# Performance work log

Hardware: AMD Instinct MI355X
Metric: run time of the kernel (lower is better)

The kernel has to match this reference:

```python
import jax, jax.numpy as jnp
import numpy as np

N = 50000        # nodes
E = 800000       # edges (avg degree 16)
IN = 256         # in_size
H = 4            # heads
C = 32           # out_size per head
NEG_SLOPE = 0.2  # PyG GATConv leaky_relu slope
LN_EPS = 1e-5


def setup_inputs() -> dict:
    key = jax.random.key(0)
    ks = jax.random.split(key, 6)
    x = jax.random.normal(ks[0], (N, IN), dtype=jnp.float32)
    edge_index = jax.random.randint(ks[1], (2, E), 0, N, dtype=jnp.int32)
    W = jax.random.normal(ks[2], (IN, H * C), dtype=jnp.float32) * 0.05
    att_src = jax.random.normal(ks[3], (H, C), dtype=jnp.float32) * 0.05
    att_dst = jax.random.normal(ks[4], (H, C), dtype=jnp.float32) * 0.05
    bias = jnp.zeros((H * C,), dtype=jnp.float32)
    ln_gamma = jnp.ones((H * C,), dtype=jnp.float32)
    ln_beta = jnp.zeros((H * C,), dtype=jnp.float32)
    return {"x": x, "edge_index": edge_index, "W": W, "att_src": att_src,
            "att_dst": att_dst, "bias": bias, "ln_gamma": ln_gamma,
            "ln_beta": ln_beta}


def _segment_softmax(alpha, seg, num_segments):
    # alpha: [E, H], softmax over edges sharing the same destination node.
    amax = jax.ops.segment_max(alpha, seg, num_segments=num_segments)  # [N, H]
    amax = jnp.where(jnp.isfinite(amax), amax, 0.0)  # nodes with no in-edges
    ex = jnp.exp(alpha - amax[seg])
    denom = jax.ops.segment_sum(ex, seg, num_segments=num_segments)    # [N, H]
    return ex / (denom[seg] + 1e-16)


def reference(x, edge_index, W, att_src, att_dst, bias, ln_gamma, ln_beta):
    # --- GATConv (concat=True) ---
    x_lin = (x @ W).reshape(N, H, C)                    # [N, H, C]
    a_src = jnp.sum(x_lin * att_src, axis=-1)           # [N, H]
    a_dst = jnp.sum(x_lin * att_dst, axis=-1)           # [N, H]
    src, dst = edge_index[0], edge_index[1]             # messages src -> dst
    alpha = a_src[src] + a_dst[dst]                     # [E, H]
    alpha = jnp.where(alpha >= 0, alpha, NEG_SLOPE * alpha)
    alpha = _segment_softmax(alpha, dst, N)             # [E, H]
    msg = x_lin[src] * alpha[..., None]                 # [E, H, C]
    out = jax.ops.segment_sum(msg, dst, num_segments=N) # [N, H, C]
    out = out.reshape(N, H * C) + bias                  # [N, H*C]
    # --- LayerNorm over feature dim ---
    mu = jnp.mean(out, axis=-1, keepdims=True)
    var = jnp.mean(jnp.square(out - mu), axis=-1, keepdims=True)
    out = (out - mu) * jax.lax.rsqrt(var + LN_EPS) * ln_gamma + ln_beta
    # --- activation ---
    return jax.nn.relu(out)
```

## Files before the change

kernel.cpp:

```cpp
#include <hip/hip_runtime.h>

#define NNODES 50000
#define NEDGES 800000
#define INFEAT 256
#define HC 128
#define NH 4
#define CPH 32
#define LSTRIDE 264
#define WSTR 68

typedef unsigned int uint32;
typedef unsigned short u16;
typedef short short8 __attribute__((ext_vector_type(8)));
typedef float f32x4 __attribute__((ext_vector_type(4)));

__device__ __forceinline__ float b2f(u16 s) {
    uint32 u = ((uint32)s) << 16;
    return __builtin_bit_cast(float, u);
}
__device__ __forceinline__ u16 f2bf(float x) {
    uint32 u = __builtin_bit_cast(uint32, x);
    uint32 r = (u + 0x7FFFu + ((u >> 16) & 1u)) >> 16;
    return (u16)r;
}
__device__ __forceinline__ bool probe_bf16(const void* gamma) {
    return ((const uint32*)gamma)[0] == 0x3F803F80u;
}
__device__ __forceinline__ float expleaky(float a) {
    return __expf(fmaxf(a, 0.2f * a));
}

__global__ __launch_bounds__(256) void wtp_kernel(const void* __restrict__ W,
                                                  const void* __restrict__ gm,
                                                  u16* __restrict__ wtp,
                                                  int* __restrict__ count) {
    const bool isbf = probe_bf16(gm);
    int c = blockIdx.x * 256 + threadIdx.x;
    if (c < 4096) {
        int kt = c >> 9, nt = (c >> 6) & 7, l = c & 63;
        int r = l & 15, quad = l >> 4;
        int n = nt * 16 + r;
        int kbase = kt * 32 + quad * 8;
        u16 vals[8];
#pragma unroll
        for (int j = 0; j < 8; ++j) {
            int k = kbase + j;
            vals[j] = isbf ? ((const u16*)W)[k * HC + n] : f2bf(((const float*)W)[k * HC + n]);
        }
        *(uint4*)(wtp + (size_t)c * 8) = *(const uint4*)vals;
    }
    uint4 z = {0u, 0u, 0u, 0u};
    uint4* cz = (uint4*)count;
    for (int i = c; i < NNODES / 4; i += 64 * 256) cz[i] = z;
}

__global__ __launch_bounds__(256) void gemm_mfma(const void* __restrict__ x,
                                                 const uint4* __restrict__ wtp,
                                                 const void* __restrict__ att_src,
                                                 const void* __restrict__ att_dst,
                                                 const void* __restrict__ gm,
                                                 u16* __restrict__ xlin,
                                                 float* __restrict__ asrc,
                                                 float* __restrict__ adst,
                                                 const int* __restrict__ ei,
                                                 int* __restrict__ count,
                                                 int* __restrict__ rank) {
    __shared__ u16 atile[4 * 16 * LSTRIDE];
    const bool isbf = probe_bf16(gm);
    const int tid = threadIdx.x;
    const int wv = tid >> 6;
    const int lane = tid & 63;
    int wave = blockIdx.x * 4 + wv;
    int r = lane & 15;
    int quad = lane >> 4;
    int m0 = wave * 16;
    u16* my = atile + wv * (16 * LSTRIDE);

    const int eb = blockIdx.x * 1024 + tid;
    int rnk[4];
    bool ev[4];
#pragma unroll
    for (int rep = 0; rep < 4; ++rep) ev[rep] = (eb + rep * 256) < NEDGES;

    if (isbf) {
        uint4 st[8];
#pragma unroll
        for (int rep = 0; rep < 8; ++rep) {
            int idx = rep * 64 + lane;
            int row = idx >> 5;
            int ch  = idx & 31;
            int gr = m0 + row;
            if (gr > NNODES - 1) gr = NNODES - 1;
            st[rep] = *(const uint4*)((const u16*)x + (size_t)gr * INFEAT + ch * 8);
        }
        int dsti[4];
#pragma unroll
        for (int rep = 0; rep < 4; ++rep)
            dsti[rep] = ev[rep] ? ei[NEDGES + eb + rep * 256] : 0;
#pragma unroll
        for (int rep = 0; rep < 4; ++rep)
            rnk[rep] = ev[rep] ? atomicAdd(&count[dsti[rep]], 1) : 0;
#pragma unroll
        for (int rep = 0; rep < 8; ++rep) {
            int idx = rep * 64 + lane;
            int row = idx >> 5;
            int ch  = idx & 31;
            *(uint4*)(my + row * LSTRIDE + ch * 8) = st[rep];
        }
    } else {
#pragma unroll
        for (int rep = 0; rep < 16; ++rep) {
            int idx = rep * 64 + lane;
            int row = idx >> 6;
            int c4  = idx & 63;
            int gr = m0 + row;
            if (gr > NNODES - 1) gr = NNODES - 1;
            float4 f = *(const float4*)((const float*)x + (size_t)gr * INFEAT + c4 * 4);
            u16 v[4] = {f2bf(f.x), f2bf(f.y), f2bf(f.z), f2bf(f.w)};
            *(uint2*)(my + row * LSTRIDE + c4 * 4) = *(const uint2*)v;
        }
        int dsti[4];
#pragma unroll
        for (int rep = 0; rep < 4; ++rep)
            dsti[rep] = ev[rep] ? ei[NEDGES + eb + rep * 256] : 0;
#pragma unroll
        for (int rep = 0; rep < 4; ++rep)
            rnk[rep] = ev[rep] ? atomicAdd(&count[dsti[rep]], 1) : 0;
    }

    f32x4 acc[8];
#pragma unroll
    for (int nt = 0; nt < 8; ++nt) acc[nt] = (f32x4){0.f, 0.f, 0.f, 0.f};

#pragma unroll
    for (int kt = 0; kt < 8; ++kt) {
        short8 afrag = __builtin_bit_cast(short8,
            *(const uint4*)(my + r * LSTRIDE + kt * 32 + quad * 8));
#pragma unroll
        for (int nt = 0; nt < 8; ++nt) {
            short8 bfrag = __builtin_bit_cast(short8, wtp[(kt * 8 + nt) * 64 + lane]);
            acc[nt] = __builtin_amdgcn_mfma_f32_16x16x32_bf16(afrag, bfrag, acc[nt], 0, 0, 0);
        }
    }
#pragma unroll
    for (int nt = 0; nt < 8; ++nt) {
#pragma unroll
        for (int reg = 0; reg < 4; ++reg) {
            int grow = m0 + quad * 4 + reg;
            if (grow < NNODES) xlin[(size_t)grow * HC + nt * 16 + r] = f2bf(acc[nt][reg]);
        }
    }

    float asv[8], adv[8];
#pragma unroll
    for (int nt = 0; nt < 8; ++nt) {
        int c = nt * 16 + r;
        if (isbf) {
            asv[nt] = b2f(((const u16*)att_src)[c]);
            adv[nt] = b2f(((const u16*)att_dst)[c]);
        } else {
            asv[nt] = ((const float*)att_src)[c];
            adv[nt] = ((const float*)att_dst)[c];
        }
    }
    float psrc[4][4], pdst[4][4];
#pragma unroll
    for (int h = 0; h < 4; ++h)
#pragma unroll
        for (int reg = 0; reg < 4; ++reg) { psrc[h][reg] = 0.f; pdst[h][reg] = 0.f; }
#pragma unroll
    for (int nt = 0; nt < 8; ++nt) {
        const int h = nt >> 1;
#pragma unroll
        for (int reg = 0; reg < 4; ++reg) {
            psrc[h][reg] = fmaf(acc[nt][reg], asv[nt], psrc[h][reg]);
            pdst[h][reg] = fmaf(acc[nt][reg], adv[nt], pdst[h][reg]);
        }
    }
#pragma unroll
    for (int m = 1; m < 16; m <<= 1) {
#pragma unroll
        for (int h = 0; h < 4; ++h)
#pragma unroll
            for (int reg = 0; reg < 4; ++reg) {
                psrc[h][reg] += __shfl_xor(psrc[h][reg], m);
                pdst[h][reg] += __shfl_xor(pdst[h][reg], m);
            }
    }
#pragma unroll
    for (int reg = 0; reg < 4; ++reg)
#pragma unroll
        for (int h = 0; h < 4; ++h)
            if (r == reg * 4 + h) {
                int grow = m0 + quad * 4 + reg;
                if (grow < NNODES) {
                    asrc[grow * 4 + h] = psrc[h][reg];
                    adst[grow * 4 + h] = pdst[h][reg];
                }
            }

#pragma unroll
    for (int rep = 0; rep < 4; ++rep)
        if (ev[rep]) rank[eb + rep * 256] = rnk[rep];
}

__global__ __launch_bounds__(256) void blkred_kernel(const int* __restrict__ count,
                                                     int* __restrict__ blksum) {
    int i = blockIdx.x * 256 + threadIdx.x;
    int v = (i < NNODES) ? count[i] : 0;
#pragma unroll
    for (int m = 1; m < 64; m <<= 1) v += __shfl_xor(v, m);
    __shared__ int s[4];
    if ((threadIdx.x & 63) == 0) s[threadIdx.x >> 6] = v;
    __syncthreads();
    if (threadIdx.x == 0) blksum[blockIdx.x] = s[0] + s[1] + s[2] + s[3];
}

__global__ __launch_bounds__(256) void scanout_kernel(const int* __restrict__ count,
                                                      const int* __restrict__ blksum,
                                                      int* __restrict__ offsets) {
    __shared__ int sb[256];
    __shared__ int sd[256];
    const int nblk = (NNODES + 255) / 256;
    int t = threadIdx.x;
    int bv = (t < nblk) ? blksum[t] : 0;
    sb[t] = bv;
    __syncthreads();
    for (int off = 1; off < 256; off <<= 1) {
        int tv = (t >= off) ? sb[t - off] : 0;
        __syncthreads();
        sb[t] += tv;
        __syncthreads();
    }
    int base = sb[blockIdx.x] - blksum[blockIdx.x];

    int i = blockIdx.x * 256 + t;
    int v = (i < NNODES) ? count[i] : 0;
    sd[t] = v;
    __syncthreads();
    for (int off = 1; off < 256; off <<= 1) {
        int tv = (t >= off) ? sd[t - off] : 0;
        __syncthreads();
        sd[t] += tv;
        __syncthreads();
    }
    if (i < NNODES) offsets[i] = base + sd[t] - v;
    if (i == 0) offsets[NNODES] = NEDGES;
}

__global__ __launch_bounds__(256) void scatter_kernel(const int* __restrict__ ei,
                                                      const int* __restrict__ offsets,
                                                      const int* __restrict__ rank,
                                                      int* __restrict__ col) {
    int e = blockIdx.x * 256 + threadIdx.x;
    if (e >= NEDGES) return;
    int d = ei[NEDGES + e];
    col[offsets[d] + rank[e]] = ei[e];
}

__global__ __launch_bounds__(256) void node_kernel(const u16* __restrict__ xlin,
                                                   const float* __restrict__ asrc,
                                                   const float* __restrict__ adst,
                                                   const int* __restrict__ offsets,
                                                   const int* __restrict__ col,
                                                   const void* __restrict__ bias,
                                                   const void* __restrict__ gamma,
                                                   const void* __restrict__ beta,
                                                   void* __restrict__ out) {
    __shared__ float wlds[4][4 * WSTR];
    __shared__ int   slds[4][64];
    const bool isbf = probe_bf16(gamma);
    const int wv = threadIdx.x >> 6;
    const int lane = threadIdx.x & 63;
    int node = blockIdx.x * 4 + wv;
    int h = lane >> 4;
    int f2 = lane * 2;
    int start = offsets[node];
    int end = offsets[node + 1];
    float4 ad4 = *(const float4*)(adst + (size_t)node * 4);

    float dsum = 0.f, acc0 = 0.f, acc1 = 0.f;
    float* wmy = wlds[wv];
    int* smy = slds[wv];

    for (int base = start; base < end; base += 64) {
        int cnt = end - base;
        if (cnt > 64) cnt = 64;
        float4 w4 = {0.f, 0.f, 0.f, 0.f};
        int src = 0;
        if (lane < cnt) {
            src = col[base + lane];
            float4 as4 = *(const float4*)(asrc + (size_t)src * 4);
            w4.x = expleaky(as4.x + ad4.x);
            w4.y = expleaky(as4.y + ad4.y);
            w4.z = expleaky(as4.z + ad4.z);
            w4.w = expleaky(as4.w + ad4.w);
        }
        smy[lane] = src;
        wmy[0 * WSTR + lane] = w4.x;
        wmy[1 * WSTR + lane] = w4.y;
        wmy[2 * WSTR + lane] = w4.z;
        wmy[3 * WSTR + lane] = w4.w;

        const float* wh = wmy + h * WSTR;
        int j = 0;
        for (; j + 7 < cnt; j += 8) {
            float4 wa = *(const float4*)(wh + j);
            float4 wb = *(const float4*)(wh + j + 4);
            int4 sa = *(const int4*)(smy + j);
            int4 sb = *(const int4*)(smy + j + 4);
            uint32 pf[8];
            pf[0] = *(const uint32*)(xlin + (size_t)sa.x * HC + f2);
            pf[1] = *(const uint32*)(xlin + (size_t)sa.y * HC + f2);
            pf[2] = *(const uint32*)(xlin + (size_t)sa.z * HC + f2);
            pf[3] = *(const uint32*)(xlin + (size_t)sa.w * HC + f2);
            pf[4] = *(const uint32*)(xlin + (size_t)sb.x * HC + f2);
            pf[5] = *(const uint32*)(xlin + (size_t)sb.y * HC + f2);
            pf[6] = *(const uint32*)(xlin + (size_t)sb.z * HC + f2);
            pf[7] = *(const uint32*)(xlin + (size_t)sb.w * HC + f2);
            float wv8[8] = {wa.x, wa.y, wa.z, wa.w, wb.x, wb.y, wb.z, wb.w};
#pragma unroll
            for (int k = 0; k < 8; ++k) {
                float w = wv8[k];
                dsum += w;
                float x0 = __builtin_bit_cast(float, pf[k] << 16);
                float x1 = __builtin_bit_cast(float, pf[k] & 0xffff0000u);
                acc0 = fmaf(x0, w, acc0);
                acc1 = fmaf(x1, w, acc1);
            }
        }
        for (; j + 3 < cnt; j += 4) {
            float4 wa = *(const float4*)(wh + j);
            int4 sa = *(const int4*)(smy + j);
            uint32 pf[4];
            pf[0] = *(const uint32*)(xlin + (size_t)sa.x * HC + f2);
            pf[1] = *(const uint32*)(xlin + (size_t)sa.y * HC + f2);
            pf[2] = *(const uint32*)(xlin + (size_t)sa.z * HC + f2);
            pf[3] = *(const uint32*)(xlin + (size_t)sa.w * HC + f2);
            float wv4[4] = {wa.x, wa.y, wa.z, wa.w};
#pragma unroll
            for (int k = 0; k < 4; ++k) {
                float w = wv4[k];
                dsum += w;
                float x0 = __builtin_bit_cast(float, pf[k] << 16);
                float x1 = __builtin_bit_cast(float, pf[k] & 0xffff0000u);
                acc0 = fmaf(x0, w, acc0);
                acc1 = fmaf(x1, w, acc1);
            }
        }
        for (; j < cnt; ++j) {
            float w = wh[j];
            int c = smy[j];
            uint32 p = *(const uint32*)(xlin + (size_t)c * HC + f2);
            dsum += w;
            float x0 = __builtin_bit_cast(float, p << 16);
            float x1 = __builtin_bit_cast(float, p & 0xffff0000u);
            acc0 = fmaf(x0, w, acc0);
            acc1 = fmaf(x1, w, acc1);
        }
    }
    float rden = 1.f / (dsum + 1e-16f);

    float bi0, bi1, g0, g1, be0, be1;
    if (isbf) {
        uint32 bb = ((const uint32*)bias)[lane];
        uint32 gg = ((const uint32*)gamma)[lane];
        uint32 eb = ((const uint32*)beta)[lane];
        bi0 = b2f((u16)(bb & 0xffffu)); bi1 = b2f((u16)(bb >> 16));
        g0  = b2f((u16)(gg & 0xffffu)); g1  = b2f((u16)(gg >> 16));
        be0 = b2f((u16)(eb & 0xffffu)); be1 = b2f((u16)(eb >> 16));
    } else {
        float2 tb = ((const float2*)bias)[lane];
        float2 tg = ((const float2*)gamma)[lane];
        float2 te = ((const float2*)beta)[lane];
        bi0 = tb.x; bi1 = tb.y; g0 = tg.x; g1 = tg.y; be0 = te.x; be1 = te.y;
    }
    float v0 = fmaf(acc0, rden, bi0);
    float v1 = fmaf(acc1, rden, bi1);
    float s2 = v0 + v1;
    float q2 = v0 * v0 + v1 * v1;
#pragma unroll
    for (int m = 1; m < 64; m <<= 1) {
        s2 += __shfl_xor(s2, m);
        q2 += __shfl_xor(q2, m);
    }
    float mean = s2 * (1.f / 128.f);
    float var = q2 * (1.f / 128.f) - mean * mean;
    float inv = rsqrtf(var + 1e-5f);
    float d0 = v0 - mean, d1 = v1 - mean;
    float o0 = fmaxf(fmaf(d0 * inv, g0, be0), 0.f);
    float o1 = fmaxf(fmaf(d1 * inv, g1, be1), 0.f);
    if (isbf) {
        uint32 po = (uint32)f2bf(o0) | ((uint32)f2bf(o1) << 16);
        ((uint32*)out)[(size_t)node * 64 + lane] = po;
    } else {
        float2 po; po.x = o0; po.y = o1;
        ((float2*)out)[(size_t)node * 64 + lane] = po;
    }
}

extern "C" void kernel_launch(void* const* d_in, const int* in_sizes, int n_in,
                              void* d_out, int out_size, void* d_ws, size_t ws_size,
                              hipStream_t stream) {
    const void* x       = d_in[0];
    const int*  ei      = (const int*)d_in[1];
    const void* W       = d_in[2];
    const void* att_src = d_in[3];
    const void* att_dst = d_in[4];
    const void* bias    = d_in[5];
    const void* gamma   = d_in[6];
    const void* beta    = d_in[7];

    char* w = (char*)d_ws;
    size_t off = 0;
    u16* xlin    = (u16*)(w + off);   off += 12800000;
    u16* wtp     = (u16*)(w + off);   off += 65536;
    float* asrc  = (float*)(w + off); off += 800000;
    float* adst  = (float*)(w + off); off += 800000;
    int* count   = (int*)(w + off);   off += 200000;
    int* offsets = (int*)(w + off);   off += 200016;
    int* rank    = (int*)(w + off);   off += 3200000;
    int* blksum  = (int*)(w + off);   off += 1024;
    int* col     = (int*)(w + off);   off += 3200000;

    const int NBLK = (NNODES + 255) / 256;
    wtp_kernel<<<64, 256, 0, stream>>>(W, gamma, wtp, count);
    gemm_mfma<<<(NNODES + 63) / 64, 256, 0, stream>>>(x, (const uint4*)wtp, att_src, att_dst,
                                                      gamma, xlin, asrc, adst,
                                                      ei, count, rank);
    blkred_kernel<<<NBLK, 256, 0, stream>>>(count, blksum);
    scanout_kernel<<<NBLK, 256, 0, stream>>>(count, blksum, offsets);
    scatter_kernel<<<(NEDGES + 255) / 256, 256, 0, stream>>>(ei, offsets, rank, col);
    node_kernel<<<NNODES / 4, 256, 0, stream>>>(xlin, asrc, adst, offsets, col,
                                                bias, gamma, beta, d_out);
}
```

Before: 209.1 us.

## Shard degree-count atomics across copies and prefetch MFMA B fragments

Edge in-degree counting now spreads its atomics over 8 per-block-shard count arrays, which are reduced with per-shard bases so the CSR scatter stays deterministic. The aim is to cut atomic contention on the shared count array. The block-sum pass is replaced by a scan in which each block recomputes its prefix by summing all preceding counts. The GEMM also prefetches the next k-step's B fragments into registers. The costs are extra memory traffic for the 8x count and base arrays, a quadratic-ish prefix-sum read, and higher register pressure.

Result: slower. 232.0 us (+11.0%).

```diff
diff --git a/kernel.cpp b/kernel.cpp
--- a/kernel.cpp
+++ b/kernel.cpp
@@ -8,6 +8,7 @@
 #define CPH 32
 #define LSTRIDE 264
 #define WSTR 68
+#define NSH 8
 
 typedef unsigned int uint32;
 typedef unsigned short u16;
@@ -33,7 +34,7 @@
 __global__ __launch_bounds__(256) void wtp_kernel(const void* __restrict__ W,
                                                   const void* __restrict__ gm,
                                                   u16* __restrict__ wtp,
-                                                  int* __restrict__ count) {
+                                                  int* __restrict__ count8) {
     const bool isbf = probe_bf16(gm);
     int c = blockIdx.x * 256 + threadIdx.x;
     if (c < 4096) {
@@ -50,8 +51,8 @@
         *(uint4*)(wtp + (size_t)c * 8) = *(const uint4*)vals;
     }
     uint4 z = {0u, 0u, 0u, 0u};
-    uint4* cz = (uint4*)count;
-    for (int i = c; i < NNODES / 4; i += 64 * 256) cz[i] = z;
+    uint4* cz = (uint4*)count8;
+    for (int i = c; i < NSH * NNODES / 4; i += 64 * 256) cz[i] = z;
 }
 
 __global__ __launch_bounds__(256) void gemm_mfma(const void* __restrict__ x,
@@ -63,7 +64,7 @@
                                                  float* __restrict__ asrc,
                                                  float* __restrict__ adst,
                                                  const int* __restrict__ ei,
-                                                 int* __restrict__ count,
+                                                 int* __restrict__ count8,
                                                  int* __restrict__ rank) {
     __shared__ u16 atile[4 * 16 * LSTRIDE];
     const bool isbf = probe_bf16(gm);
@@ -75,6 +76,7 @@
     int quad = lane >> 4;
     int m0 = wave * 16;
     u16* my = atile + wv * (16 * LSTRIDE);
+    int* mycnt = count8 + (blockIdx.x & (NSH - 1)) * NNODES;
 
     const int eb = blockIdx.x * 1024 + tid;
     int rnk[4];
@@ -99,7 +101,7 @@
             dsti[rep] = ev[rep] ? ei[NEDGES + eb + rep * 256] : 0;
 #pragma unroll
         for (int rep = 0; rep < 4; ++rep)
-            rnk[rep] = ev[rep] ? atomicAdd(&count[dsti[rep]], 1) : 0;
+            rnk[rep] = ev[rep] ? atomicAdd(&mycnt[dsti[rep]], 1) : 0;
 #pragma unroll
         for (int rep = 0; rep < 8; ++rep) {
             int idx = rep * 64 + lane;
@@ -125,23 +127,33 @@
             dsti[rep] = ev[rep] ? ei[NEDGES + eb + rep * 256] : 0;
 #pragma unroll
         for (int rep = 0; rep < 4; ++rep)
-            rnk[rep] = ev[rep] ? atomicAdd(&count[dsti[rep]], 1) : 0;
+            rnk[rep] = ev[rep] ? atomicAdd(&mycnt[dsti[rep]], 1) : 0;
     }
 
     f32x4 acc[8];
 #pragma unroll
     for (int nt = 0; nt < 8; ++nt) acc[nt] = (f32x4){0.f, 0.f, 0.f, 0.f};
 
+    short8 bcur[8], bnext[8];
+#pragma unroll
+    for (int nt = 0; nt < 8; ++nt)
+        bcur[nt] = __builtin_bit_cast(short8, wtp[nt * 64 + lane]);
 #pragma unroll
     for (int kt = 0; kt < 8; ++kt) {
+        if (kt < 7) {
+#pragma unroll
+            for (int nt = 0; nt < 8; ++nt)
+                bnext[nt] = __builtin_bit_cast(short8, wtp[((kt + 1) * 8 + nt) * 64 + lane]);
+        }
         short8 afrag = __builtin_bit_cast(short8,
             *(const uint4*)(my + r * LSTRIDE + kt * 32 + quad * 8));
 #pragma unroll
-        for (int nt = 0; nt < 8; ++nt) {
-            short8 bfrag = __builtin_bit_cast(short8, wtp[(kt * 8 + nt) * 64 + lane]);
-            acc[nt] = __builtin_amdgcn_mfma_f32_16x16x32_bf16(afrag, bfrag, acc[nt], 0, 0, 0);
-        }
-    }
+        for (int nt = 0; nt < 8; ++nt)
+            acc[nt] = __builtin_amdgcn_mfma_f32_16x16x32_bf16(afrag, bcur[nt], acc[nt], 0, 0, 0);
+#pragma unroll
+        for (int nt = 0; nt < 8; ++nt) bcur[nt] = bnext[nt];
+    }
+
 #pragma unroll
     for (int nt = 0; nt < 8; ++nt) {
 #pragma unroll
@@ -204,37 +216,35 @@
         if (ev[rep]) rank[eb + rep * 256] = rnk[rep];
 }
 
-__global__ __launch_bounds__(256) void blkred_kernel(const int* __restrict__ count,
-                                                     int* __restrict__ blksum) {
-    int i = blockIdx.x * 256 + threadIdx.x;
-    int v = (i < NNODES) ? count[i] : 0;
-#pragma unroll
-    for (int m = 1; m < 64; m <<= 1) v += __shfl_xor(v, m);
-    __shared__ int s[4];
-    if ((threadIdx.x & 63) == 0) s[threadIdx.x >> 6] = v;
+__global__ __launch_bounds__(256) void cred_kernel(const int* __restrict__ count8,
+                                                   int* __restrict__ count,
+                                                   int* __restrict__ base8) {
+    int n = blockIdx.x * 256 + threadIdx.x;
+    if (n >= NNODES) return;
+    int acc = 0;
+#pragma unroll
+    for (int s = 0; s < NSH; ++s) {
+        base8[(size_t)s * NNODES + n] = acc;
+        acc += count8[(size_t)s * NNODES + n];
+    }
+    count[n] = acc;
+}
+
+__global__ __launch_bounds__(256) void scanout_kernel(const int* __restrict__ count,
+                                                      int* __restrict__ offsets) {
+    __shared__ int sd[256];
+    __shared__ int sw[4];
+    const int t = threadIdx.x;
+    const int lim = blockIdx.x * 256;
+    int p = 0;
+    for (int i = t; i < lim; i += 256) p += count[i];
+#pragma unroll
+    for (int m = 1; m < 64; m <<= 1) p += __shfl_xor(p, m);
+    if ((t & 63) == 0) sw[t >> 6] = p;
     __syncthreads();
-    if (threadIdx.x == 0) blksum[blockIdx.x] = s[0] + s[1] + s[2] + s[3];
-}
-
-__global__ __launch_bounds__(256) void scanout_kernel(const int* __restrict__ count,
-                                                      const int* __restrict__ blksum,
-                                                      int* __restrict__ offsets) {
-    __shared__ int sb[256];
-    __shared__ int sd[256];
-    const int nblk = (NNODES + 255) / 256;
-    int t = threadIdx.x;
-    int bv = (t < nblk) ? blksum[t] : 0;
-    sb[t] = bv;
-    __syncthreads();
-    for (int off = 1; off < 256; off <<= 1) {
-        int tv = (t >= off) ? sb[t - off] : 0;
-        __syncthreads();
-        sb[t] += tv;
-        __syncthreads();
-    }
-    int base = sb[blockIdx.x] - blksum[blockIdx.x];
-
-    int i = blockIdx.x * 256 + t;
+    int base = sw[0] + sw[1] + sw[2] + sw[3];
+
+    int i = lim + t;
     int v = (i < NNODES) ? count[i] : 0;
     sd[t] = v;
     __syncthreads();
@@ -250,12 +260,14 @@
 
 __global__ __launch_bounds__(256) void scatter_kernel(const int* __restrict__ ei,
                                                       const int* __restrict__ offsets,
+                                                      const int* __restrict__ base8,
                                                       const int* __restrict__ rank,
                                                       int* __restrict__ col) {
     int e = blockIdx.x * 256 + threadIdx.x;
     if (e >= NEDGES) return;
     int d = ei[NEDGES + e];
-    col[offsets[d] + rank[e]] = ei[e];
+    int s = (e >> 10) & (NSH - 1);
+    col[offsets[d] + base8[(size_t)s * NNODES + d] + rank[e]] = ei[e];
 }
 
 __global__ __launch_bounds__(256) void node_kernel(const u16* __restrict__ xlin,
@@ -417,20 +429,21 @@
     u16* wtp     = (u16*)(w + off);   off += 65536;
     float* asrc  = (float*)(w + off); off += 800000;
     float* adst  = (float*)(w + off); off += 800000;
+    int* count8  = (int*)(w + off);   off += (size_t)NSH * NNODES * 4;
     int* count   = (int*)(w + off);   off += 200000;
+    int* base8   = (int*)(w + off);   off += (size_t)NSH * NNODES * 4;
     int* offsets = (int*)(w + off);   off += 200016;
     int* rank    = (int*)(w + off);   off += 3200000;
-    int* blksum  = (int*)(w + off);   off += 1024;
     int* col     = (int*)(w + off);   off += 3200000;
 
     const int NBLK = (NNODES + 255) / 256;
-    wtp_kernel<<<64, 256, 0, stream>>>(W, gamma, wtp, count);
+    wtp_kernel<<<64, 256, 0, stream>>>(W, gamma, wtp, count8);
     gemm_mfma<<<(NNODES + 63) / 64, 256, 0, stream>>>(x, (const uint4*)wtp, att_src, att_dst,
                                                       gamma, xlin, asrc, adst,
-                                                      ei, count, rank);
-    blkred_kernel<<<NBLK, 256, 0, stream>>>(count, blksum);
-    scanout_kernel<<<NBLK, 256, 0, stream>>>(count, blksum, offsets);
-    scatter_kernel<<<(NEDGES + 255) / 256, 256, 0, stream>>>(ei, offsets, rank, col);
+                                                      ei, count8, rank);
+    cred_kernel<<<NBLK, 256, 0, stream>>>(count8, count, base8);
+    scanout_kernel<<<NBLK, 256, 0, stream>>>(count, offsets);
+    scatter_kernel<<<(NEDGES + 255) / 256, 256, 0, stream>>>(ei, offsets, base8, rank, col);
     node_kernel<<<NNODES / 4, 256, 0, stream>>>(xlin, asrc, adst, offsets, col,
                                                 bias, gamma, beta, d_out);
 }
```

## Fuse scan, scatter and node stages into one cooperative kernel with grid syncs

Applied to the files above, without the earlier changes.

Replaces the four post-GEMM launches (block reduce, scan, CSR scatter, node aggregation) with a single cooperative persistent kernel that uses grid.sync between phases. Grid size comes from occupancy queries, capped at 2048 blocks, and the old multi-launch path remains as a fallback. The GEMM also now prefetches the next k-tile of B fragments into registers. The aim is to cut launch and tail overhead between small dependent kernels. In exchange it adds grid-wide barrier cost, lower occupancy limits for the node phase, and extra register pressure in the GEMM.

Result: slower. 470.5 us (+125.0%).

```diff
diff --git a/kernel.cpp b/kernel.cpp
--- a/kernel.cpp
+++ b/kernel.cpp
@@ -1,4 +1,7 @@
 #include <hip/hip_runtime.h>
+#include <hip/hip_cooperative_groups.h>
+
+namespace cg = cooperative_groups;
 
 #define NNODES 50000
 #define NEDGES 800000
@@ -8,6 +11,7 @@
 #define CPH 32
 #define LSTRIDE 264
 #define WSTR 68
+#define NBLK 196
 
 typedef unsigned int uint32;
 typedef unsigned short u16;
@@ -132,16 +136,26 @@
 #pragma unroll
     for (int nt = 0; nt < 8; ++nt) acc[nt] = (f32x4){0.f, 0.f, 0.f, 0.f};
 
+    short8 bcur[8], bnext[8];
+#pragma unroll
+    for (int nt = 0; nt < 8; ++nt)
+        bcur[nt] = __builtin_bit_cast(short8, wtp[nt * 64 + lane]);
 #pragma unroll
     for (int kt = 0; kt < 8; ++kt) {
+        if (kt < 7) {
+#pragma unroll
+            for (int nt = 0; nt < 8; ++nt)
+                bnext[nt] = __builtin_bit_cast(short8, wtp[((kt + 1) * 8 + nt) * 64 + lane]);
+        }
         short8 afrag = __builtin_bit_cast(short8,
             *(const uint4*)(my + r * LSTRIDE + kt * 32 + quad * 8));
 #pragma unroll
-        for (int nt = 0; nt < 8; ++nt) {
-            short8 bfrag = __builtin_bit_cast(short8, wtp[(kt * 8 + nt) * 64 + lane]);
-            acc[nt] = __builtin_amdgcn_mfma_f32_16x16x32_bf16(afrag, bfrag, acc[nt], 0, 0, 0);
-        }
-    }
+        for (int nt = 0; nt < 8; ++nt)
+            acc[nt] = __builtin_amdgcn_mfma_f32_16x16x32_bf16(afrag, bcur[nt], acc[nt], 0, 0, 0);
+#pragma unroll
+        for (int nt = 0; nt < 8; ++nt) bcur[nt] = bnext[nt];
+    }
+
 #pragma unroll
     for (int nt = 0; nt < 8; ++nt) {
 #pragma unroll
@@ -204,26 +218,25 @@
         if (ev[rep]) rank[eb + rep * 256] = rnk[rep];
 }
 
-__global__ __launch_bounds__(256) void blkred_kernel(const int* __restrict__ count,
-                                                     int* __restrict__ blksum) {
-    int i = blockIdx.x * 256 + threadIdx.x;
+
+__device__ __forceinline__ void blkred_body(const int* __restrict__ count,
+                                            int* __restrict__ blksum, int blk,
+                                            int t, int* s4) {
+    int i = blk * 256 + t;
     int v = (i < NNODES) ? count[i] : 0;
 #pragma unroll
     for (int m = 1; m < 64; m <<= 1) v += __shfl_xor(v, m);
-    __shared__ int s[4];
-    if ((threadIdx.x & 63) == 0) s[threadIdx.x >> 6] = v;
+    if ((t & 63) == 0) s4[t >> 6] = v;
     __syncthreads();
-    if (threadIdx.x == 0) blksum[blockIdx.x] = s[0] + s[1] + s[2] + s[3];
-}
-
-__global__ __launch_bounds__(256) void scanout_kernel(const int* __restrict__ count,
-                                                      const int* __restrict__ blksum,
-                                                      int* __restrict__ offsets) {
-    __shared__ int sb[256];
-    __shared__ int sd[256];
-    const int nblk = (NNODES + 255) / 256;
-    int t = threadIdx.x;
-    int bv = (t < nblk) ? blksum[t] : 0;
+    if (t == 0) blksum[blk] = s4[0] + s4[1] + s4[2] + s4[3];
+    __syncthreads();
+}
+
+__device__ __forceinline__ void scanout_body(const int* __restrict__ count,
+                                             const int* __restrict__ blksum,
+                                             int* __restrict__ offsets, int blk,
+                                             int t, int* sb, int* sd) {
+    int bv = (t < NBLK) ? blksum[t] : 0;
     sb[t] = bv;
     __syncthreads();
     for (int off = 1; off < 256; off <<= 1) {
@@ -232,9 +245,9 @@
         sb[t] += tv;
         __syncthreads();
     }
-    int base = sb[blockIdx.x] - blksum[blockIdx.x];
-
-    int i = blockIdx.x * 256 + t;
+    int base = sb[blk] - blksum[blk];
+
+    int i = blk * 256 + t;
     int v = (i < NNODES) ? count[i] : 0;
     sd[t] = v;
     __syncthreads();
@@ -246,33 +259,20 @@
     }
     if (i < NNODES) offsets[i] = base + sd[t] - v;
     if (i == 0) offsets[NNODES] = NEDGES;
-}
-
-__global__ __launch_bounds__(256) void scatter_kernel(const int* __restrict__ ei,
-                                                      const int* __restrict__ offsets,
-                                                      const int* __restrict__ rank,
-                                                      int* __restrict__ col) {
-    int e = blockIdx.x * 256 + threadIdx.x;
-    if (e >= NEDGES) return;
-    int d = ei[NEDGES + e];
-    col[offsets[d] + rank[e]] = ei[e];
-}
-
-__global__ __launch_bounds__(256) void node_kernel(const u16* __restrict__ xlin,
-                                                   const float* __restrict__ asrc,
-                                                   const float* __restrict__ adst,
-                                                   const int* __restrict__ offsets,
-                                                   const int* __restrict__ col,
-                                                   const void* __restrict__ bias,
-                                                   const void* __restrict__ gamma,
-                                                   const void* __restrict__ beta,
-                                                   void* __restrict__ out) {
-    __shared__ float wlds[4][4 * WSTR];
-    __shared__ int   slds[4][64];
-    const bool isbf = probe_bf16(gamma);
-    const int wv = threadIdx.x >> 6;
-    const int lane = threadIdx.x & 63;
-    int node = blockIdx.x * 4 + wv;
+    __syncthreads();
+}
+
+__device__ __forceinline__ void node_body(const u16* __restrict__ xlin,
+                                          const float* __restrict__ asrc,
+                                          const float* __restrict__ adst,
+                                          const int* __restrict__ offsets,
+                                          const int* __restrict__ col,
+                                          const void* __restrict__ bias,
+                                          const void* __restrict__ gamma,
+                                          const void* __restrict__ beta,
+                                          void* __restrict__ out,
+                                          bool isbf, int node, int lane,
+                                          float* wmy, int* smy) {
     int h = lane >> 4;
     int f2 = lane * 2;
     int start = offsets[node];
@@ -280,8 +280,6 @@
     float4 ad4 = *(const float4*)(adst + (size_t)node * 4);
 
     float dsum = 0.f, acc0 = 0.f, acc1 = 0.f;
-    float* wmy = wlds[wv];
-    int* smy = slds[wv];
 
     for (int base = start; base < end; base += 64) {
         int cnt = end - base;
@@ -399,6 +397,94 @@
     }
 }
 
+__global__ __launch_bounds__(256) void mega_kernel(const int* __restrict__ ei,
+                                                   const int* __restrict__ count,
+                                                   int* __restrict__ blksum,
+                                                   int* __restrict__ offsets,
+                                                   const int* __restrict__ rank,
+                                                   int* __restrict__ col,
+                                                   const u16* __restrict__ xlin,
+                                                   const float* __restrict__ asrc,
+                                                   const float* __restrict__ adst,
+                                                   const void* __restrict__ bias,
+                                                   const void* __restrict__ gamma,
+                                                   const void* __restrict__ beta,
+                                                   void* __restrict__ out) {
+    __shared__ int s4[4];
+    __shared__ int sb[256];
+    __shared__ int sd[256];
+    __shared__ float wlds[4][4 * WSTR];
+    __shared__ int   slds[4][64];
+
+    cg::grid_group grid = cg::this_grid();
+    const int t = threadIdx.x;
+    const int nb = gridDim.x;
+    const bool isbf = probe_bf16(gamma);
+
+    for (int blk = blockIdx.x; blk < NBLK; blk += nb)
+        blkred_body(count, blksum, blk, t, s4);
+    grid.sync();
+
+    for (int blk = blockIdx.x; blk < NBLK; blk += nb)
+        scanout_body(count, blksum, offsets, blk, t, sb, sd);
+    grid.sync();
+
+    for (int e = blockIdx.x * 256 + t; e < NEDGES; e += nb * 256) {
+        int d = ei[NEDGES + e];
+        col[offsets[d] + rank[e]] = ei[e];
+    }
+    grid.sync();
+
+    const int wv = t >> 6;
+    const int lane = t & 63;
+    float* wmy = wlds[wv];
+    int* smy = slds[wv];
+    const int nwaves = nb * 4;
+    for (int node = blockIdx.x * 4 + wv; node < NNODES; node += nwaves)
+        node_body(xlin, asrc, adst, offsets, col, bias, gamma, beta, out,
+                  isbf, node, lane, wmy, smy);
+}
+
+__global__ __launch_bounds__(256) void blkred_kernel(const int* __restrict__ count,
+                                                     int* __restrict__ blksum) {
+    __shared__ int s4[4];
+    blkred_body(count, blksum, blockIdx.x, threadIdx.x, s4);
+}
+__global__ __launch_bounds__(256) void scanout_kernel(const int* __restrict__ count,
+                                                      const int* __restrict__ blksum,
+                                                      int* __restrict__ offsets) {
+    __shared__ int sb[256];
+    __shared__ int sd[256];
+    scanout_body(count, blksum, offsets, blockIdx.x, threadIdx.x, sb, sd);
+}
+__global__ __launch_bounds__(256) void scatter_kernel(const int* __restrict__ ei,
+                                                      const int* __restrict__ offsets,
+                                                      const int* __restrict__ rank,
+                                                      int* __restrict__ col) {
+    int e = blockIdx.x * 256 + threadIdx.x;
+    if (e >= NEDGES) return;
+    int d = ei[NEDGES + e];
+    col[offsets[d] + rank[e]] = ei[e];
+}
+__global__ __launch_bounds__(256) void node_kernel(const u16* __restrict__ xlin,
+                                                   const float* __restrict__ asrc,
+                                                   const float* __restrict__ adst,
+                                                   const int* __restrict__ offsets,
+                                                   const int* __restrict__ col,
+                                                   const void* __restrict__ bias,
+                                                   const void* __restrict__ gamma,
+                                                   const void* __restrict__ beta,
+                                                   void* __restrict__ out) {
+    __shared__ float wlds[4][4 * WSTR];
+    __shared__ int   slds[4][64];
+    const bool isbf = probe_bf16(gamma);
+    const int wv = threadIdx.x >> 6;
+    const int lane = threadIdx.x & 63;
+    int node = blockIdx.x * 4 + wv;
+    node_body(xlin, asrc, adst, offsets, col, bias, gamma, beta, out,
+              isbf, node, lane, wlds[wv], slds[wv]);
+}
+
 extern "C" void kernel_launch(void* const* d_in, const int* in_sizes, int n_in,
                               void* d_out, int out_size, void* d_ws, size_t ws_size,
                               hipStream_t stream) {
@@ -423,14 +509,38 @@
     int* blksum  = (int*)(w + off);   off += 1024;
     int* col     = (int*)(w + off);   off += 3200000;
 
-    const int NBLK = (NNODES + 255) / 256;
+    static int mega_grid = -2;
+    if (mega_grid == -2) {
+        int bpc = 0;
+        hipError_t err = hipOccupancyMaxActiveBlocksPerMultiprocessor(
+            &bpc, mega_kernel, 256, 0);
+        if (err == hipSuccess && bpc > 0) {
+            int g = bpc * 256;
+            if (g > 2048) g = 2048;
+            mega_grid = g;
+        } else {
+            mega_grid = -1;
+        }
+    }
+
     wtp_kernel<<<64, 256, 0, stream>>>(W, gamma, wtp, count);
     gemm_mfma<<<(NNODES + 63) / 64, 256, 0, stream>>>(x, (const uint4*)wtp, att_src, att_dst,
                                                       gamma, xlin, asrc, adst,
                                                       ei, count, rank);
-    blkred_kernel<<<NBLK, 256, 0, stream>>>(count, blksum);
-    scanout_kernel<<<NBLK, 256, 0, stream>>>(count, blksum, offsets);
-    scatter_kernel<<<(NEDGES + 255) / 256, 256, 0, stream>>>(ei, offsets, rank, col);
-    node_kernel<<<NNODES / 4, 256, 0, stream>>>(xlin, asrc, adst, offsets, col,
-                                                bias, gamma, beta, d_out);
-}
+    if (mega_grid > 0) {
+        const u16* xl = xlin; const float* as = asrc; const float* ad = adst;
+        const int* ofs = offsets; const int* rk = rank;
+        void* outp = d_out;
+        void* args[] = {(void*)&ei, (void*)&count, (void*)&blksum, (void*)&ofs,
+                        (void*)&rk, (void*)&col, (void*)&xl, (void*)&as, (void*)&ad,
+                        (void*)&bias, (void*)&gamma, (void*)&beta, (void*)&outp};
+        hipLaunchCooperativeKernel((void*)mega_kernel, dim3(mega_grid), dim3(256),
+                                   args, 0, stream);
+    } else {
+        blkred_kernel<<<NBLK, 256, 0, stream>>>(count, blksum);
+        scanout_kernel<<<NBLK, 256, 0, stream>>>(count, blksum, offsets);
+        scatter_kernel<<<(NEDGES + 255) / 256, 256, 0, stream>>>(ei, offsets, rank, col);
+        node_kernel<<<NNODES / 4, 256, 0, stream>>>(xlin, asrc, adst, offsets, col,
+                                                    bias, gamma, beta, d_out);
+    }
+}
```
